# Kernel tuning notes

Measured on AMD Instinct MI355X. Metric: run time of the kernel, lower is better.

## Reference

```python
import jax, jax.numpy as jnp
import numpy as np

B, T, C, H, W = 2, 16, 128, 32, 32
D_STATE, D_CONV, EXPAND = 16, 4, 2
D_INNER = EXPAND * C           # 256
DT_RANK = (C + 15) // 16       # 8 (mamba default ceil(d_model/16))
HIDDEN = int(C * 4.0)          # mlp_ratio = 4
EPS = 1e-6


def setup_inputs() -> dict:
    key = jax.random.key(0)
    ks = jax.random.split(key, 10)
    f = lambda k, s, sc=0.02: jax.random.normal(k, s, jnp.float32) * sc
    return dict(
        x=jax.random.normal(ks[0], (B, T, C, H, W), jnp.float32),
        norm1_w=jnp.ones((C,), jnp.float32),
        in_proj_w=f(ks[1], (2 * D_INNER, C)),
        conv_w=f(ks[2], (D_INNER, D_CONV), 0.1),
        conv_b=jnp.zeros((D_INNER,), jnp.float32),
        x_proj_w=f(ks[3], (DT_RANK + 2 * D_STATE, D_INNER)),
        dt_proj_w=f(ks[4], (D_INNER, DT_RANK), 0.1),
        dt_proj_b=jnp.full((D_INNER,), -2.0, jnp.float32),
        A_log=jnp.log(jnp.tile(jnp.arange(1, D_STATE + 1, dtype=jnp.float32), (D_INNER, 1))),
        D_param=jnp.ones((D_INNER,), jnp.float32),
        out_proj_w=f(ks[5], (C, D_INNER)),
        norm2_w=jnp.ones((C,), jnp.float32),
        fc1_w=f(ks[6], (HIDDEN, C)),
        fc1_b=jnp.zeros((HIDDEN,), jnp.float32),
        fc2_w=f(ks[7], (C, HIDDEN)),
        fc2_b=jnp.zeros((C,), jnp.float32),
    )


def _rmsnorm(x, w):
    var = jnp.mean(x * x, axis=-1, keepdims=True)
    return w * (x * jax.lax.rsqrt(var + EPS))


def _mamba(x, in_proj_w, conv_w, conv_b, x_proj_w, dt_proj_w, dt_proj_b,
           A_log, D_param, out_proj_w):
    # x: [Bn, T, C]
    Bn, T_, _ = x.shape
    xz = jnp.einsum('btc,ec->bte', x, in_proj_w)        # [Bn,T,2*Di]
    xi, z = jnp.split(xz, 2, axis=-1)
    # causal depthwise conv1d over T (kernel size D_CONV)
    xp = jnp.pad(xi, ((0, 0), (D_CONV - 1, 0), (0, 0)))
    conv = conv_b + sum(xp[:, k:k + T_, :] * conv_w[:, k] for k in range(D_CONV))
    xc = jax.nn.silu(conv)                               # [Bn,T,Di]
    dbl = jnp.einsum('btd,ed->bte', xc, x_proj_w)
    dt, Bm, Cm = jnp.split(dbl, [DT_RANK, DT_RANK + D_STATE], axis=-1)
    dt = jax.nn.softplus(jnp.einsum('btr,dr->btd', dt, dt_proj_w) + dt_proj_b)
    A = -jnp.exp(A_log)                                  # [Di,S]

    def step(h, inp):
        dt_t, B_t, C_t, u_t = inp                        # [Bn,Di],[Bn,S],[Bn,S],[Bn,Di]
        dA = jnp.exp(dt_t[:, :, None] * A)               # [Bn,Di,S]
        h = h * dA + dt_t[:, :, None] * B_t[:, None, :] * u_t[:, :, None]
        y = jnp.einsum('bds,bs->bd', h, C_t) + D_param * u_t
        return h, y

    h0 = jnp.zeros((Bn, D_INNER, D_STATE), x.dtype)
    xs = (dt.transpose(1, 0, 2), Bm.transpose(1, 0, 2),
          Cm.transpose(1, 0, 2), xc.transpose(1, 0, 2))
    _, ys = jax.lax.scan(step, h0, xs)                   # [T,Bn,Di]
    y = ys.transpose(1, 0, 2) * jax.nn.silu(z)
    return jnp.einsum('btd,cd->btc', y, out_proj_w)


def reference(x, norm1_w, in_proj_w, conv_w, conv_b, x_proj_w, dt_proj_w,
              dt_proj_b, A_log, D_param, out_proj_w, norm2_w,
              fc1_w, fc1_b, fc2_w, fc2_b):
    Bb, Tt, Cc, Hh, Ww = x.shape
    x_t = x.transpose(0, 3, 4, 1, 2).reshape(Bb * Hh * Ww, Tt, Cc)
    x_norm = _rmsnorm(x_t, norm1_w)
    m_args = (in_proj_w, conv_w, conv_b, x_proj_w, dt_proj_w, dt_proj_b,
              A_log, D_param, out_proj_w)
    out_fwd = _mamba(x_norm, *m_args)
    out_bwd = jnp.flip(_mamba(jnp.flip(x_norm, 1), *m_args), 1)
    x_t = x_t + out_fwd + out_bwd
    h = jax.nn.gelu(jnp.einsum('btc,hc->bth', _rmsnorm(x_t, norm2_w), fc1_w) + fc1_b,
                    approximate=False)
    mlp_out = jnp.einsum('bth,ch->btc', h, fc2_w) + fc2_b
    x_t = x_t + mlp_out
    return x_t.reshape(Bb, Hh, Ww, Tt, Cc).transpose(0, 3, 4, 1, 2)
```

## Files before the change

kernel.cpp:

```cpp
#include <hip/hip_runtime.h>
#include <math.h>

#define TT   16
#define CC   128
#define DI   256
#define SS   16
#define RR   8
#define HID  512
#define HWW  1024
#define NB   2048
#define EPSF 1e-6f

#define OFF_INPROJ  0
#define OFF_XPROJ   65536
#define OFF_OUTPROJ 75776
#define OFF_FC1     108544
#define OFF_FC2     174080
#define W_TOTAL     239616

#define WSB_XCF  524288u
#define WSB_XCB  (524288u + 16777216u)
#define WSB_Z    (524288u + 33554432u)
#define WS_NEEDED (524288u + 50331648u)

using f32x4  = __attribute__((ext_vector_type(4))) float;
using short8 = __attribute__((ext_vector_type(8))) short;

#define MFMA(a, b, c) __builtin_amdgcn_mfma_f32_16x16x32_bf16((a), (b), (c), 0, 0, 0)

__device__ __forceinline__ float siluf(float x) {
    return x * __builtin_amdgcn_rcpf(1.0f + __expf(-x));
}
__device__ __forceinline__ float geluf(float x) {
    float y = 0.7978845608028654f * (x + 0.044715f * x * x * x);
    y = fminf(y, 15.f);
    float e = __expf(2.f * y);
    float t = (e - 1.f) * __builtin_amdgcn_rcpf(e + 1.f);
    return 0.5f * x * (1.f + t);
}
__device__ __forceinline__ short f2bf(float f) {
    unsigned u = __float_as_uint(f);
    u += 0x7fffu + ((u >> 16) & 1u);
    return (short)(u >> 16);
}
__device__ __forceinline__ float bf2f(short s) {
    return __uint_as_float(((unsigned)(unsigned short)s) << 16);
}
__device__ __forceinline__ void stbf(char* base, int row, int col, int rowbytes, float v) {
    int byte = (col * 2) ^ ((row & 7) << 4);
    *(short*)(base + row * rowbytes + byte) = f2bf(v);
}
__device__ __forceinline__ float ldbf(const char* base, int row, int col, int rowbytes) {
    int byte = (col * 2) ^ ((row & 7) << 4);
    return bf2f(*(const short*)(base + row * rowbytes + byte));
}
__device__ __forceinline__ short ldraw(const char* base, int row, int col, int rowbytes) {
    int byte = (col * 2) ^ ((row & 7) << 4);
    return *(const short*)(base + row * rowbytes + byte);
}
__device__ __forceinline__ short8 ldA(const char* base, int row, int kelem, int rowbytes) {
    int byte = (kelem * 2) ^ ((row & 7) << 4);
    return *(const short8*)(base + row * rowbytes + byte);
}
__device__ __forceinline__ short8 ldB(const short* base, int idx) {
    return *(const short8*)(base + idx);
}

__global__ __launch_bounds__(256)
void cvt_weights(const float* __restrict__ in_proj_w,
                 const float* __restrict__ x_proj_w,
                 const float* __restrict__ out_proj_w,
                 const float* __restrict__ fc1_w,
                 const float* __restrict__ fc2_w,
                 short* __restrict__ ws)
{
    int i4 = (blockIdx.x * 256 + threadIdx.x) * 4;
    if (i4 >= W_TOTAL) return;
    const float* src;
    int off;
    if      (i4 < OFF_XPROJ)   { src = in_proj_w;  off = OFF_INPROJ;  }
    else if (i4 < OFF_OUTPROJ) { src = x_proj_w;   off = OFF_XPROJ;   }
    else if (i4 < OFF_FC1)     { src = out_proj_w; off = OFF_OUTPROJ; }
    else if (i4 < OFF_FC2)     { src = fc1_w;      off = OFF_FC1;     }
    else                       { src = fc2_w;      off = OFF_FC2;     }
    float4 v = *(const float4*)(src + (i4 - off));
    short4 o;
    o.x = f2bf(v.x); o.y = f2bf(v.y); o.z = f2bf(v.z); o.w = f2bf(v.w);
    *(short4*)(ws + i4) = o;
}

__global__ __launch_bounds__(256, 6)
void ka_front(const float* __restrict__ x,
              const float* __restrict__ norm1_w,
              const float* __restrict__ conv_w,
              const float* __restrict__ conv_b,
              const short* __restrict__ bw_in,
              short* __restrict__ xcf_g,
              short* __restrict__ xcb_g,
              short* __restrict__ z_g)
{
    __shared__ __align__(16) char lds[20480];
    char* A0 = lds;
    char* A1 = lds + 8192;
    char* A2 = lds + 12288;

    const int tid  = threadIdx.x;
    const int lane = tid & 63, wave = tid >> 6;
    const int mrow = lane & 15, kgrp = lane >> 4;
    const int n  = ((blockIdx.x & 7) << 8) | (blockIdx.x >> 3);
    const int b  = n >> 10, hw = n & 1023;
    const float* xin = x + (size_t)b * TT * CC * HWW + hw;

    {
        float* sX = (float*)A0;
        #pragma unroll
        for (int i = 0; i < 8; ++i) { int idx = tid + i * 256; sX[idx] = xin[(size_t)idx * HWW]; }
    }
    __syncthreads();
    {
        const float* sX = (const float*)A0;
        const int row = tid >> 4, l16 = tid & 15;
        float v[8]; float ssum = 0.f;
        #pragma unroll
        for (int k = 0; k < 8; ++k) { v[k] = sX[row * CC + l16 + 16 * k]; ssum += v[k] * v[k]; }
        ssum += __shfl_xor(ssum, 1); ssum += __shfl_xor(ssum, 2);
        ssum += __shfl_xor(ssum, 4); ssum += __shfl_xor(ssum, 8);
        const float rstd = __builtin_amdgcn_rsqf(ssum * (1.0f / CC) + EPSF);
        #pragma unroll
        for (int k = 0; k < 8; ++k) {
            int c = l16 + 16 * k;
            stbf(A1, row, c, 256, v[k] * rstd * norm1_w[c]);
        }
    }
    __syncthreads();
    {
        short8 aF[4];
        #pragma unroll
        for (int k = 0; k < 4; ++k) aF[k] = ldA(A1, mrow, k * 32 + kgrp * 8, 256);
        char* dst = (wave < 2) ? A0 : A2;
        const int n_w = wave * 128;
        #pragma unroll
        for (int q = 0; q < 4; ++q) {
            const int c0 = n_w + q * 32 + mrow;
            short8 b0[4], b1[4];
            #pragma unroll
            for (int k = 0; k < 4; ++k) b0[k] = ldB(bw_in, c0 * CC + kgrp * 8 + k * 32);
            #pragma unroll
            for (int k = 0; k < 4; ++k) b1[k] = ldB(bw_in, (c0 + 16) * CC + kgrp * 8 + k * 32);
            f32x4 a0 = (f32x4){0.f, 0.f, 0.f, 0.f};
            f32x4 a1 = (f32x4){0.f, 0.f, 0.f, 0.f};
            #pragma unroll
            for (int k = 0; k < 4; ++k) { a0 = MFMA(aF[k], b0[k], a0); a1 = MFMA(aF[k], b1[k], a1); }
            const int cl0 = c0 & 255, cl1 = (c0 + 16) & 255;
            #pragma unroll
            for (int r = 0; r < 4; ++r) {
                stbf(dst, kgrp * 4 + r, cl0, 512, a0[r]);
                stbf(dst, kgrp * 4 + r, cl1, 512, a1[r]);
            }
        }
    }
    __syncthreads();
    {
        const int ch = tid;
        float xi_r[TT];
        #pragma unroll
        for (int t = 0; t < TT; ++t) xi_r[t] = ldbf(A0, t, ch, 512);
        const float4 cw = *(const float4*)(conv_w + ch * 4);
        const float  cb = conv_b[ch];
        short* xf = xcf_g + n * 4096 + ch;
        short* xb = xcb_g + n * 4096 + ch;
        short* zo = z_g   + n * 4096 + ch;
        #pragma unroll
        for (int t = 0; t < TT; ++t) {
            float vf = fmaf(cw.w, xi_r[t], cb);
            if (t >= 1) vf = fmaf(cw.z, xi_r[t - 1], vf);
            if (t >= 2) vf = fmaf(cw.y, xi_r[t - 2], vf);
            if (t >= 3) vf = fmaf(cw.x, xi_r[t - 3], vf);
            xf[t * 256] = f2bf(siluf(vf));
            float vb = fmaf(cw.w, xi_r[15 - t], cb);
            if (t >= 1) vb = fmaf(cw.z, xi_r[16 - t], vb);
            if (t >= 2) vb = fmaf(cw.y, xi_r[17 - t], vb);
            if (t >= 3) vb = fmaf(cw.x, xi_r[18 - t], vb);
            xb[t * 256] = f2bf(siluf(vb));
            zo[t * 256] = ldraw(A2, t, ch, 512);
        }
    }
}

__global__ __launch_bounds__(256, 5)
void kb_scan(const float* __restrict__ dt_proj_w,
             const float* __restrict__ dt_proj_b,
             const float* __restrict__ D_param,
             const short* __restrict__ bw_xp,
             short* __restrict__ xcf_g,
             short* __restrict__ xcb_g,
             const short* __restrict__ z_g)
{
    __shared__ __align__(16) char lds[19456];
    char*  L0 = lds;
    char*  L1 = lds + 8192;
    float* SD = (float*)(lds + 16384);

    const int tid  = threadIdx.x;
    const int lane = tid & 63, wave = tid >> 6;
    const int mrow = lane & 15, kgrp = lane >> 4;
    const int dir = blockIdx.x & 1;
    const int bsw = blockIdx.x >> 1;
    const int n = ((bsw & 7) << 8) | (bsw >> 3);
    short* xcn = (dir ? xcb_g : xcf_g) + n * 4096;
    const short* zn = z_g + n * 4096;

    {
        #pragma unroll
        for (int p = 0; p < 2; ++p) {
            int i8 = tid + p * 256;
            int e = i8 * 8, row = e >> 8, col = e & 255;
            short8 v = *(const short8*)(xcn + e);
            short8 w = *(const short8*)(zn + e);
            int byte = (col * 2) ^ ((row & 7) << 4);
            *(short8*)(L0 + row * 512 + byte) = v;
            *(short8*)(L1 + row * 512 + byte) = w;
        }
    }
    __syncthreads();
    {
        if (wave < 3) {
            const int col  = wave * 16 + mrow;
            const int colc = (col < 40) ? col : 39;
            short8 bF[8];
            #pragma unroll
            for (int k = 0; k < 8; ++k) bF[k] = ldB(bw_xp, colc * DI + k * 32 + kgrp * 8);
            f32x4 aE = (f32x4){0.f, 0.f, 0.f, 0.f};
            f32x4 aO = (f32x4){0.f, 0.f, 0.f, 0.f};
            #pragma unroll
            for (int k = 0; k < 4; ++k) {
                aE = MFMA(ldA(L0, mrow, (2 * k)     * 32 + kgrp * 8, 512), bF[2 * k],     aE);
                aO = MFMA(ldA(L0, mrow, (2 * k + 1) * 32 + kgrp * 8, 512), bF[2 * k + 1], aO);
            }
            if (col < 40) {
                #pragma unroll
                for (int r = 0; r < 4; ++r) SD[(kgrp * 4 + r) * 40 + col] = aE[r] + aO[r];
            }
        }
    }
    __syncthreads();
    {
        const int ch = tid;
        float dtw[RR];
        {
            float4 w0 = *(const float4*)(dt_proj_w + ch * RR);
            float4 w1 = *(const float4*)(dt_proj_w + ch * RR + 4);
            dtw[0] = w0.x; dtw[1] = w0.y; dtw[2] = w0.z; dtw[3] = w0.w;
            dtw[4] = w1.x; dtw[5] = w1.y; dtw[6] = w1.z; dtw[7] = w1.w;
        }
        const float db_ = dt_proj_b[ch];
        const float Dp  = D_param[ch];
        float u[TT];
        #pragma unroll
        for (int t = 0; t < TT; ++t) u[t] = ldbf(L0, t, ch, 512);
        float h[SS];
        #pragma unroll
        for (int s = 0; s < SS; ++s) h[s] = 0.f;
        #pragma unroll
        for (int t = 0; t < TT; ++t) {
            float xr = db_;
            #pragma unroll
            for (int r = 0; r < RR; ++r) xr = fmaf(dtw[r], SD[t * 40 + r], xr);
            const float e  = __expf(xr);
            const float dt = (xr > 15.f) ? xr : __logf(1.f + e);
            const int   to = dir ? (15 - t) : t;
            const float zv = ldbf(L1, to, ch, 512);
            float dA[SS];
            dA[0] = __builtin_amdgcn_rcpf(1.f + e);
            #pragma unroll
            for (int i = 1; i < SS; ++i) dA[i] = dA[(i - 1) >> 1] * dA[i >> 1];
            const float bu = dt * u[t];
            float y = 0.f;
            #pragma unroll
            for (int sg = 0; sg < 4; ++sg) {
                f32x4 B4 = *(const f32x4*)(SD + t * 40 + 8  + sg * 4);
                f32x4 C4 = *(const f32x4*)(SD + t * 40 + 24 + sg * 4);
                h[sg*4+0] = fmaf(h[sg*4+0], dA[sg*4+0], B4[0] * bu); y = fmaf(h[sg*4+0], C4[0], y);
                h[sg*4+1] = fmaf(h[sg*4+1], dA[sg*4+1], B4[1] * bu); y = fmaf(h[sg*4+1], C4[1], y);
                h[sg*4+2] = fmaf(h[sg*4+2], dA[sg*4+2], B4[2] * bu); y = fmaf(h[sg*4+2], C4[2], y);
                h[sg*4+3] = fmaf(h[sg*4+3], dA[sg*4+3], B4[3] * bu); y = fmaf(h[sg*4+3], C4[3], y);
            }
            y = fmaf(Dp, u[t], y) * siluf(zv);
            xcn[t * 256 + ch] = f2bf(y);
        }
    }
}

__global__ __launch_bounds__(256, 4)
void kc_back2(const float* __restrict__ x,
              const float* __restrict__ norm2_w,
              const float* __restrict__ fc1_b,
              const float* __restrict__ fc2_b,
              const short* __restrict__ bw,
              const short* __restrict__ yf_g,
              const short* __restrict__ yb_g,
              float* __restrict__ out)
{
    __shared__ __align__(16) char lds[40960];
    float* X2 = (float*)lds;
    char*  A1 = lds + 16384;
    char*  H  = lds + 24576;

    const short* bw_op = bw + OFF_OUTPROJ;
    const short* bw_f1 = bw + OFF_FC1;
    const short* bw_f2 = bw + OFF_FC2;

    const int tid  = threadIdx.x;
    const int lane = tid & 63, wave = tid >> 6;
    const int mrow = lane & 15, kgrp = lane >> 4;
    const int bsw = ((blockIdx.x & 7) << 7) | (blockIdx.x >> 3);
    const int n0 = bsw * 2, n1 = n0 + 1;
    const int b0 = n0 >> 10, hw0 = n0 & 1023;
    const int b1 = n1 >> 10, hw1 = n1 & 1023;
    const float* xin0 = x + (size_t)b0 * TT * CC * HWW + hw0;
    const float* xin1 = x + (size_t)b1 * TT * CC * HWW + hw1;
    float* oout0 = out + (size_t)b0 * TT * CC * HWW + hw0;
    float* oout1 = out + (size_t)b1 * TT * CC * HWW + hw1;

    float* X2A = X2;
    float* X2B = X2 + 2048;
    const int c0 = wave * 32 + mrow;
    const int c1 = c0 + 16;

    {
        float xrA[8], xrB[8];
        #pragma unroll
        for (int r = 0; r < 4; ++r) {
            const int row = kgrp * 4 + r;
            xrA[r]     = xin0[(size_t)(row * CC + c0) * HWW];
            xrA[4 + r] = xin0[(size_t)(row * CC + c1) * HWW];
            xrB[r]     = xin1[(size_t)(row * CC + c0) * HWW];
            xrB[4 + r] = xin1[(size_t)(row * CC + c1) * HWW];
        }
        const short* yfA = yf_g + n0 * 4096;
        const short* yfB = yf_g + n1 * 4096;
        const short* ybA = yb_g + n0 * 4096;
        const short* ybB = yb_g + n1 * 4096;
        f32x4 a0A = (f32x4){0.f,0.f,0.f,0.f}, a1A = a0A, a0B = a0A, a1B = a0A;
        #pragma unroll 2
        for (int kk = 0; kk < 8; ++kk) {
            const int ko = kk * 32 + kgrp * 8;
            short8 bF0 = ldB(bw_op, c0 * DI + ko);
            short8 bF1 = ldB(bw_op, c1 * DI + ko);
            short8 fA = *(const short8*)(yfA + mrow * 256 + ko);
            short8 fB = *(const short8*)(yfB + mrow * 256 + ko);
            short8 gA = *(const short8*)(ybA + (15 - mrow) * 256 + ko);
            short8 gB = *(const short8*)(ybB + (15 - mrow) * 256 + ko);
            a0A = MFMA(fA, bF0, a0A); a0A = MFMA(gA, bF0, a0A);
            a1A = MFMA(fA, bF1, a1A); a1A = MFMA(gA, bF1, a1A);
            a0B = MFMA(fB, bF0, a0B); a0B = MFMA(gB, bF0, a0B);
            a1B = MFMA(fB, bF1, a1B); a1B = MFMA(gB, bF1, a1B);
        }
        #pragma unroll
        for (int r = 0; r < 4; ++r) {
            const int row = kgrp * 4 + r;
            X2A[row * CC + c0] = a0A[r] + xrA[r];
            X2A[row * CC + c1] = a1A[r] + xrA[4 + r];
            X2B[row * CC + c0] = a0B[r] + xrB[r];
            X2B[row * CC + c1] = a1B[r] + xrB[4 + r];
        }
    }
    __syncthreads();

    {
        const int row = tid >> 3;
        const int s   = row >> 4;
        const int r16 = row & 15;
        const int l8  = tid & 7;
        const float* Xs = X2 + s * 2048;
        float v[16]; float ssum = 0.f;
        #pragma unroll
        for (int k = 0; k < 16; ++k) { v[k] = Xs[r16 * CC + l8 + 8 * k]; ssum += v[k] * v[k]; }
        ssum += __shfl_xor(ssum, 1); ssum += __shfl_xor(ssum, 2); ssum += __shfl_xor(ssum, 4);
        const float rstd = __builtin_amdgcn_rsqf(ssum * (1.0f / CC) + EPSF);
        char* A1s = A1 + s * 4096;
        #pragma unroll
        for (int k = 0; k < 16; ++k) {
            int c = l8 + 8 * k;
            stbf(A1s, r16, c, 256, v[k] * rstd * norm2_w[c]);
        }
    }
    __syncthreads();

    {
        short8 aFA[4], aFB[4];
        #pragma unroll
        for (int k = 0; k < 4; ++k) {
            aFA[k] = ldA(A1,        mrow, k * 32 + kgrp * 8, 256);
            aFB[k] = ldA(A1 + 4096, mrow, k * 32 + kgrp * 8, 256);
        }
        f32x4 o0A = (f32x4){0.f,0.f,0.f,0.f}, o1A = o0A, o0B = o0A, o1B = o0A;
        #pragma unroll
        for (int hh = 0; hh < 2; ++hh) {
            #pragma unroll
            for (int q = 0; q < 2; ++q) {
                const int cc0 = hh * 256 + wave * 64 + q * 32 + mrow;
                const int cc1 = cc0 + 16;
                f32x4 h0A = (f32x4){0.f,0.f,0.f,0.f}, h1A = h0A, h0B = h0A, h1B = h0A;
                #pragma unroll
                for (int k = 0; k < 4; ++k) {
                    short8 b0 = ldB(bw_f1, cc0 * CC + kgrp * 8 + k * 32);
                    short8 b1 = ldB(bw_f1, cc1 * CC + kgrp * 8 + k * 32);
                    h0A = MFMA(aFA[k], b0, h0A); h1A = MFMA(aFA[k], b1, h1A);
                    h0B = MFMA(aFB[k], b0, h0B); h1B = MFMA(aFB[k], b1, h1B);
                }
                const float bb0 = fc1_b[cc0], bb1 = fc1_b[cc1];
                const int cl0 = cc0 & 255, cl1 = cc1 & 255;
                #pragma unroll
                for (int r = 0; r < 4; ++r) {
                    stbf(H,        kgrp * 4 + r, cl0, 512, geluf(h0A[r] + bb0));
                    stbf(H,        kgrp * 4 + r, cl1, 512, geluf(h1A[r] + bb1));
                    stbf(H + 8192, kgrp * 4 + r, cl0, 512, geluf(h0B[r] + bb0));
                    stbf(H + 8192, kgrp * 4 + r, cl1, 512, geluf(h1B[r] + bb1));
                }
            }
            __syncthreads();
            #pragma unroll 2
            for (int k = 0; k < 8; ++k) {
                const int ko = k * 32 + kgrp * 8;
                short8 b0 = ldB(bw_f2, c0 * HID + hh * 256 + ko);
                short8 b1 = ldB(bw_f2, c1 * HID + hh * 256 + ko);
                short8 aA = ldA(H,        mrow, ko, 512);
                short8 aB = ldA(H + 8192, mrow, ko, 512);
                o0A = MFMA(aA, b0, o0A); o1A = MFMA(aA, b1, o1A);
                o0B = MFMA(aB, b0, o0B); o1B = MFMA(aB, b1, o1B);
            }
            __syncthreads();
        }
        const float bb0 = fc2_b[c0], bb1 = fc2_b[c1];
        #pragma unroll
        for (int r = 0; r < 4; ++r) {
            const int row = kgrp * 4 + r;
            oout0[(size_t)(row * CC + c0) * HWW] = X2A[row * CC + c0] + o0A[r] + bb0;
            oout0[(size_t)(row * CC + c1) * HWW] = X2A[row * CC + c1] + o1A[r] + bb1;
            oout1[(size_t)(row * CC + c0) * HWW] = X2B[row * CC + c0] + o0B[r] + bb0;
            oout1[(size_t)(row * CC + c1) * HWW] = X2B[row * CC + c1] + o1B[r] + bb1;
        }
    }
}

template<int DIR>
__device__ __forceinline__ void scan_mono(const float* __restrict__ dbl,
                                          char* __restrict__ xcb,
                                          const char* __restrict__ zb,
                                          char* __restrict__ yb,
                                          const float* __restrict__ dtw,
                                          float db_, float Dp, int ch)
{
    float u[TT];
    #pragma unroll
    for (int t = 0; t < TT; ++t) u[t] = ldbf(xcb, t, ch, 512);
    float h[SS];
    #pragma unroll
    for (int s = 0; s < SS; ++s) h[s] = 0.f;
    #pragma unroll
    for (int t = 0; t < TT; ++t) {
        float xr = db_;
        #pragma unroll
        for (int r = 0; r < RR; ++r) xr = fmaf(dtw[r], dbl[t * 40 + r], xr);
        const float e  = __expf(xr);
        const float dt = (xr > 15.f) ? xr : __logf(1.f + e);
        const int   to = DIR ? (15 - t) : t;
        const float zv = ldbf(zb, to, ch, 512);
        float dA[SS];
        dA[0] = __builtin_amdgcn_rcpf(1.f + e);
        #pragma unroll
        for (int i = 1; i < SS; ++i) dA[i] = dA[(i - 1) >> 1] * dA[i >> 1];
        const float bu = dt * u[t];
        float y = 0.f;
        #pragma unroll
        for (int sg = 0; sg < 4; ++sg) {
            float4 B4 = *(const float4*)(dbl + t * 40 + 8  + sg * 4);
            float4 C4 = *(const float4*)(dbl + t * 40 + 24 + sg * 4);
            h[sg*4+0] = fmaf(h[sg*4+0], dA[sg*4+0], B4.x * bu); y = fmaf(h[sg*4+0], C4.x, y);
            h[sg*4+1] = fmaf(h[sg*4+1], dA[sg*4+1], B4.y * bu); y = fmaf(h[sg*4+1], C4.y, y);
            h[sg*4+2] = fmaf(h[sg*4+2], dA[sg*4+2], B4.z * bu); y = fmaf(h[sg*4+2], C4.z, y);
            h[sg*4+3] = fmaf(h[sg*4+3], dA[sg*4+3], B4.w * bu); y = fmaf(h[sg*4+3], C4.w, y);
        }
        y = fmaf(Dp, u[t], y) * siluf(zv);
        if (DIR == 0) stbf(xcb, t,  ch, 512, y);
        else          stbf(yb,  to, ch, 512, y);
    }
}

__global__ __launch_bounds__(512, 4)
void tmb_mono(const float* __restrict__ x,
              const float* __restrict__ norm1_w,
              const float* __restrict__ conv_w,
              const float* __restrict__ conv_b,
              const float* __restrict__ dt_proj_w,
              const float* __restrict__ dt_proj_b,
              const float* __restrict__ D_param,
              const float* __restrict__ norm2_w,
              const float* __restrict__ fc1_b,
              const float* __restrict__ fc2_b,
              const short* __restrict__ bw,
              float* __restrict__ out)
{
    __shared__ __align__(16) char lds[40960];
    char* A0  = lds;
    char* A2  = lds + 8192;
    char* A3  = lds + 16384;
    char* A4f = lds + 24576;
    char* A4b = lds + 32768;

    const short* bw_in = bw + OFF_INPROJ;
    const short* bw_xp = bw + OFF_XPROJ;
    const short* bw_op = bw + OFF_OUTPROJ;
    const short* bw_f1 = bw + OFF_FC1;
    const short* bw_f2 = bw + OFF_FC2;

    const int tid  = threadIdx.x;
    const int team = tid >> 8;
    const int ch   = tid & 255;
    const int lane = tid & 63;
    const int wave = tid >> 6;
    const int mrow = lane & 15;
    const int kgrp = lane >> 4;

    const int n  = ((blockIdx.x & 7) << 8) | (blockIdx.x >> 3);
    const int b  = n >> 10;
    const int hw = n & 1023;
    const float* xin  = x   + (size_t)b * TT * CC * HWW + hw;
    float*       oout = out + (size_t)b * TT * CC * HWW + hw;

    {
        float* sX = (float*)A0;
        #pragma unroll
        for (int i = 0; i < 4; ++i) { int idx = tid + i * 512; sX[idx] = xin[(size_t)idx * HWW]; }
    }
    __syncthreads();
    float res[4];
    {
        const float* sX = (const float*)A0;
        #pragma unroll
        for (int i = 0; i < 4; ++i) res[i] = sX[tid + i * 512];
    }
    {
        const float* sX = (const float*)A0;
        const int row = tid >> 5, l32 = tid & 31;
        float v[4]; float ssum = 0.f;
        #pragma unroll
        for (int k = 0; k < 4; ++k) { v[k] = sX[row * CC + l32 + 32 * k]; ssum += v[k] * v[k]; }
        ssum += __shfl_xor(ssum, 1); ssum += __shfl_xor(ssum, 2);
        ssum += __shfl_xor(ssum, 4); ssum += __shfl_xor(ssum, 8); ssum += __shfl_xor(ssum, 16);
        const float rstd = __builtin_amdgcn_rsqf(ssum * (1.0f / CC) + EPSF);
        #pragma unroll
        for (int k = 0; k < 4; ++k) { int c = l32 + 32 * k; stbf(A4f, row, c, 256, v[k] * rstd * norm1_w[c]); }
    }
    __syncthreads();
    {
        short8 aF[4];
        #pragma unroll
        for (int k = 0; k < 4; ++k) aF[k] = ldA(A4f, mrow, k * 32 + kgrp * 8, 256);
        const int n_w = wave * 64;
        short8 bX[8], bY[8];
        #pragma unroll
        for (int i = 0; i < 8; ++i) { const int tile = i >> 2, k = i & 3; bX[i] = ldB(bw_in, (n_w + tile * 16 + mrow) * CC + kgrp * 8 + k * 32); }
        #pragma unroll
        for (int i = 0; i < 8; ++i) { const int tile = 2 + (i >> 2), k = i & 3; bY[i] = ldB(bw_in, (n_w + tile * 16 + mrow) * CC + kgrp * 8 + k * 32); }
        f32x4 acc[4];
        #pragma unroll
        for (int i = 0; i < 4; ++i) acc[i] = (f32x4){0.f, 0.f, 0.f, 0.f};
        #pragma unroll
        for (int i = 0; i < 8; ++i) acc[i >> 2]       = MFMA(aF[i & 3], bX[i], acc[i >> 2]);
        #pragma unroll
        for (int i = 0; i < 8; ++i) acc[2 + (i >> 2)] = MFMA(aF[i & 3], bY[i], acc[2 + (i >> 2)]);
        char* dst = (wave < 4) ? A2 : A3;
        #pragma unroll
        for (int tile = 0; tile < 4; ++tile) {
            const int cl = (n_w + tile * 16 + mrow) & 255;
            #pragma unroll
            for (int r = 0; r < 4; ++r) stbf(dst, kgrp * 4 + r, cl, 512, acc[tile][r]);
        }
    }
    __syncthreads();
    {
        float xi_r[TT];
        #pragma unroll
        for (int t = 0; t < TT; ++t) xi_r[t] = ldbf(A2, t, ch, 512);
        const float4 cw = *(const float4*)(conv_w + ch * 4);
        const float  cb = conv_b[ch];
        char* dst = team ? A4b : A4f;
        if (team == 0) {
            #pragma unroll
            for (int t = 0; t < TT; ++t) {
                float vf = fmaf(cw.w, xi_r[t], cb);
                if (t >= 1) vf = fmaf(cw.z, xi_r[t - 1], vf);
                if (t >= 2) vf = fmaf(cw.y, xi_r[t - 2], vf);
                if (t >= 3) vf = fmaf(cw.x, xi_r[t - 3], vf);
                stbf(dst, t, ch, 512, siluf(vf));
            }
        } else {
            #pragma unroll
            for (int t = 0; t < TT; ++t) {
                float vb = fmaf(cw.w, xi_r[15 - t], cb);
                if (t >= 1) vb = fmaf(cw.z, xi_r[16 - t], vb);
                if (t >= 2) vb = fmaf(cw.y, xi_r[17 - t], vb);
                if (t >= 3) vb = fmaf(cw.x, xi_r[18 - t], vb);
                stbf(dst, t, ch, 512, siluf(vb));
            }
        }
    }
    __syncthreads();
    float* SDBL = (float*)A0;
    {
        const int wv = wave & 3;
        if (wv < 3) {
            const char* src = team ? A4b : A4f;
            float* db = SDBL + team * 640;
            const int col  = wv * 16 + mrow;
            const int colc = (col < 40) ? col : 39;
            const int wp = colc * DI + kgrp * 8;
            short8 bF[8];
            #pragma unroll
            for (int k = 0; k < 8; ++k) bF[k] = ldB(bw_xp, wp + k * 32);
            f32x4 accE = (f32x4){0.f, 0.f, 0.f, 0.f};
            f32x4 accO = (f32x4){0.f, 0.f, 0.f, 0.f};
            #pragma unroll
            for (int k = 0; k < 4; ++k) {
                accE = MFMA(ldA(src, mrow, (2*k)   * 32 + kgrp * 8, 512), bF[2*k],   accE);
                accO = MFMA(ldA(src, mrow, (2*k+1) * 32 + kgrp * 8, 512), bF[2*k+1], accO);
            }
            if (col < 40) {
                #pragma unroll
                for (int r = 0; r < 4; ++r) db[(kgrp * 4 + r) * 40 + col] = accE[r] + accO[r];
            }
        }
    }
    __syncthreads();
    {
        float dtw[RR];
        float4 w0 = *(const float4*)(dt_proj_w + ch * RR);
        float4 w1 = *(const float4*)(dt_proj_w + ch * RR + 4);
        dtw[0] = w0.x; dtw[1] = w0.y; dtw[2] = w0.z; dtw[3] = w0.w;
        dtw[4] = w1.x; dtw[5] = w1.y; dtw[6] = w1.z; dtw[7] = w1.w;
        const float db_ = dt_proj_b[ch];
        const float Dp  = D_param[ch];
        if (team == 0) scan_mono<0>(SDBL,       A4f, A3, A4f, dtw, db_, Dp, ch);
        else           scan_mono<1>(SDBL + 640, A4b, A3, A2,  dtw, db_, Dp, ch);
    }
    __syncthreads();
    {
        const int col = wave * 16 + mrow;
        short8 bF[8];
        #pragma unroll
        for (int k = 0; k < 8; ++k) bF[k] = ldB(bw_op, col * DI + k * 32 + kgrp * 8);
        f32x4 accE = (f32x4){0.f, 0.f, 0.f, 0.f};
        f32x4 accO = (f32x4){0.f, 0.f, 0.f, 0.f};
        #pragma unroll
        for (int k = 0; k < 4; ++k) {
            accE = MFMA(ldA(A4f, mrow, (2*k)   * 32 + kgrp * 8, 512), bF[2*k],   accE);
            accO = MFMA(ldA(A4f, mrow, (2*k+1) * 32 + kgrp * 8, 512), bF[2*k+1], accO);
        }
        #pragma unroll
        for (int k = 0; k < 4; ++k) {
            accE = MFMA(ldA(A2, mrow, (2*k)   * 32 + kgrp * 8, 512), bF[2*k],   accE);
            accO = MFMA(ldA(A2, mrow, (2*k+1) * 32 + kgrp * 8, 512), bF[2*k+1], accO);
        }
        float* O = (float*)A3;
        #pragma unroll
        for (int r = 0; r < 4; ++r) O[(kgrp * 4 + r) * CC + col] = accE[r] + accO[r];
    }
    __syncthreads();
    {
        const float* O  = (const float*)A3;
        float*       X2 = (float*)A0;
        #pragma unroll
        for (int i = 0; i < 4; ++i) { int idx = tid + i * 512; X2[idx] = res[i] + O[idx]; }
    }
    __syncthreads();
    {
        const float* sX = (const float*)A0;
        const int row = tid >> 5, l32 = tid & 31;
        float v[4]; float ssum = 0.f;
        #pragma unroll
        for (int k = 0; k < 4; ++k) { v[k] = sX[row * CC + l32 + 32 * k]; ssum += v[k] * v[k]; }
        ssum += __shfl_xor(ssum, 1); ssum += __shfl_xor(ssum, 2);
        ssum += __shfl_xor(ssum, 4); ssum += __shfl_xor(ssum, 8); ssum += __shfl_xor(ssum, 16);
        const float rstd = __builtin_amdgcn_rsqf(ssum * (1.0f / CC) + EPSF);
        #pragma unroll
        for (int k = 0; k < 4; ++k) { int c = l32 + 32 * k; stbf(A4f, row, c, 256, v[k] * rstd * norm2_w[c]); }
    }
    __syncthreads();
    {
        short8 aF[4];
        #pragma unroll
        for (int k = 0; k < 4; ++k) aF[k] = ldA(A4f, mrow, k * 32 + kgrp * 8, 256);
        const int n_w = wave * 64;
        short8 bX[8], bY[8];
        #pragma unroll
        for (int i = 0; i < 8; ++i) { const int tile = i >> 2, k = i & 3; bX[i] = ldB(bw_f1, (n_w + tile * 16 + mrow) * CC + kgrp * 8 + k * 32); }
        #pragma unroll
        for (int i = 0; i < 8; ++i) { const int tile = 2 + (i >> 2), k = i & 3; bY[i] = ldB(bw_f1, (n_w + tile * 16 + mrow) * CC + kgrp * 8 + k * 32); }
        f32x4 acc[4];
        #pragma unroll
        for (int i = 0; i < 4; ++i) acc[i] = (f32x4){0.f, 0.f, 0.f, 0.f};
        #pragma unroll
        for (int i = 0; i < 8; ++i) acc[i >> 2]       = MFMA(aF[i & 3], bX[i], acc[i >> 2]);
        #pragma unroll
        for (int i = 0; i < 8; ++i) acc[2 + (i >> 2)] = MFMA(aF[i & 3], bY[i], acc[2 + (i >> 2)]);
        char* dst = (wave < 4) ? A2 : A3;
        #pragma unroll
        for (int tile = 0; tile < 4; ++tile) {
            const int col = n_w + tile * 16 + mrow;
            const float b1 = fc1_b[col];
            const int cl = col & 255;
            #pragma unroll
            for (int r = 0; r < 4; ++r) stbf(dst, kgrp * 4 + r, cl, 512, geluf(acc[tile][r] + b1));
        }
    }
    __syncthreads();
    {
        const int col = wave * 16 + mrow;
        short8 bX[8], bY[8];
        #pragma unroll
        for (int k = 0; k < 8; ++k) bX[k] = ldB(bw_f2, col * HID + k * 32 + kgrp * 8);
        #pragma unroll
        for (int k = 0; k < 8; ++k) bY[k] = ldB(bw_f2, col * HID + (8 + k) * 32 + kgrp * 8);
        f32x4 accE = (f32x4){0.f, 0.f, 0.f, 0.f};
        f32x4 accO = (f32x4){0.f, 0.f, 0.f, 0.f};
        #pragma unroll
        for (int k = 0; k < 8; ++k) {
            accE = MFMA(ldA(A2, mrow, k * 32 + kgrp * 8, 512), bX[k], accE);
            accO = MFMA(ldA(A3, mrow, k * 32 + kgrp * 8, 512), bY[k], accO);
        }
        const float* X2 = (const float*)A0;
        const float bb = fc2_b[col];
        #pragma unroll
        for (int r = 0; r < 4; ++r) {
            const int t = kgrp * 4 + r;
            oout[(size_t)(t * CC + col) * HWW] = X2[t * CC + col] + accE[r] + accO[r] + bb;
        }
    }
}

extern "C" void kernel_launch(void* const* d_in, const int* in_sizes, int n_in,
                              void* d_out, int out_size, void* d_ws, size_t ws_size,
                              hipStream_t stream) {
    (void)in_sizes; (void)n_in; (void)out_size;
    short* bw = (short*)d_ws;
    cvt_weights<<<dim3((W_TOTAL / 4 + 255) / 256), dim3(256), 0, stream>>>(
        (const float*)d_in[2],  (const float*)d_in[5],  (const float*)d_in[10],
        (const float*)d_in[12], (const float*)d_in[14], bw);

    if (ws_size >= (size_t)WS_NEEDED) {
        short* xcf = (short*)((char*)d_ws + WSB_XCF);
        short* xcb = (short*)((char*)d_ws + WSB_XCB);
        short* zg  = (short*)((char*)d_ws + WSB_Z);
        ka_front<<<dim3(NB), dim3(256), 0, stream>>>(
            (const float*)d_in[0], (const float*)d_in[1], (const float*)d_in[3],
            (const float*)d_in[4], bw + OFF_INPROJ, xcf, xcb, zg);
        kb_scan<<<dim3(NB * 2), dim3(256), 0, stream>>>(
            (const float*)d_in[6], (const float*)d_in[7], (const float*)d_in[9],
            bw + OFF_XPROJ, xcf, xcb, zg);
        kc_back2<<<dim3(NB / 2), dim3(256), 0, stream>>>(
            (const float*)d_in[0], (const float*)d_in[11], (const float*)d_in[13],
            (const float*)d_in[15], bw, xcf, xcb, (float*)d_out);
    } else {
        tmb_mono<<<dim3(NB), dim3(512), 0, stream>>>(
            (const float*)d_in[0],  (const float*)d_in[1],  (const float*)d_in[3],
            (const float*)d_in[4],  (const float*)d_in[6],  (const float*)d_in[7],
            (const float*)d_in[9],  (const float*)d_in[11], (const float*)d_in[13],
            (const float*)d_in[15], bw, (float*)d_out);
    }
}
```

Measured before the change: 181.6 us.

## Stage residual and output in contiguous workspace, add tiled transpose kernel for output

The front kernel now also writes the raw input per sequence into a contiguous fp32 workspace buffer. The back kernel reads the residual from that buffer instead of doing strided gathers, and writes its result contiguously into a buffer that reuses the z region. A new LDS-tiled transpose kernel then scatters that buffer into the final strided output layout with coalesced float4 accesses. The goal is to replace strided global reads and writes with coalesced ones, at the cost of extra workspace traffic and one more kernel launch; the scan kernel's block-to-direction mapping is also reordered.

```diff
diff --git a/kernel.cpp b/kernel.cpp
--- a/kernel.cpp
+++ b/kernel.cpp
@@ -18,10 +18,12 @@
 #define OFF_FC2     174080
 #define W_TOTAL     239616
 
-#define WSB_XCF  524288u
-#define WSB_XCB  (524288u + 16777216u)
-#define WSB_Z    (524288u + 33554432u)
-#define WS_NEEDED (524288u + 50331648u)
+#define WSB_XCF   524288u
+#define WSB_XCB   (524288u + 16777216u)
+#define WSB_ZXO   (524288u + 33554432u)
+#define WSB_XRES  (524288u + 50331648u)
+#define WS_T1     (524288u + 50331648u)
+#define WS_T2     (524288u + 67108864u)
 
 using f32x4  = __attribute__((ext_vector_type(4))) float;
 using short8 = __attribute__((ext_vector_type(8))) short;
@@ -89,6 +91,7 @@
     *(short4*)(ws + i4) = o;
 }
 
+template<int XRES>
 __global__ __launch_bounds__(256, 6)
 void ka_front(const float* __restrict__ x,
               const float* __restrict__ norm1_w,
@@ -97,7 +100,8 @@
               const short* __restrict__ bw_in,
               short* __restrict__ xcf_g,
               short* __restrict__ xcb_g,
-              short* __restrict__ z_g)
+              short* __restrict__ z_g,
+              float* __restrict__ xres_g)
 {
     __shared__ __align__(16) char lds[20480];
     char* A0 = lds;
@@ -114,7 +118,12 @@
     {
         float* sX = (float*)A0;
         #pragma unroll
-        for (int i = 0; i < 8; ++i) { int idx = tid + i * 256; sX[idx] = xin[(size_t)idx * HWW]; }
+        for (int i = 0; i < 8; ++i) {
+            int idx = tid + i * 256;
+            float v = xin[(size_t)idx * HWW];
+            sX[idx] = v;
+            if (XRES) xres_g[(size_t)n * 2048 + idx] = v;
+        }
     }
     __syncthreads();
     {
@@ -204,8 +213,8 @@
     const int tid  = threadIdx.x;
     const int lane = tid & 63, wave = tid >> 6;
     const int mrow = lane & 15, kgrp = lane >> 4;
-    const int dir = blockIdx.x & 1;
-    const int bsw = blockIdx.x >> 1;
+    const int dir = blockIdx.x >> 11;
+    const int bsw = blockIdx.x & 2047;
     const int n = ((bsw & 7) << 8) | (bsw >> 3);
     short* xcn = (dir ? xcb_g : xcf_g) + n * 4096;
     const short* zn = z_g + n * 4096;
@@ -291,15 +300,17 @@
     }
 }
 
+template<int XRES>
 __global__ __launch_bounds__(256, 4)
 void kc_back2(const float* __restrict__ x,
+              const float* __restrict__ xres,
               const float* __restrict__ norm2_w,
               const float* __restrict__ fc1_b,
               const float* __restrict__ fc2_b,
               const short* __restrict__ bw,
               const short* __restrict__ yf_g,
               const short* __restrict__ yb_g,
-              float* __restrict__ out)
+              float* __restrict__ xout)
 {
     __shared__ __align__(16) char lds[40960];
     float* X2 = (float*)lds;
@@ -319,8 +330,8 @@
     const int b1 = n1 >> 10, hw1 = n1 & 1023;
     const float* xin0 = x + (size_t)b0 * TT * CC * HWW + hw0;
     const float* xin1 = x + (size_t)b1 * TT * CC * HWW + hw1;
-    float* oout0 = out + (size_t)b0 * TT * CC * HWW + hw0;
-    float* oout1 = out + (size_t)b1 * TT * CC * HWW + hw1;
+    float* xoA = xout + (size_t)n0 * 2048;
+    float* xoB = xout + (size_t)n1 * 2048;
 
     float* X2A = X2;
     float* X2B = X2 + 2048;
@@ -329,13 +340,26 @@
 
     {
         float xrA[8], xrB[8];
-        #pragma unroll
-        for (int r = 0; r < 4; ++r) {
-            const int row = kgrp * 4 + r;
-            xrA[r]     = xin0[(size_t)(row * CC + c0) * HWW];
-            xrA[4 + r] = xin0[(size_t)(row * CC + c1) * HWW];
-            xrB[r]     = xin1[(size_t)(row * CC + c0) * HWW];
-            xrB[4 + r] = xin1[(size_t)(row * CC + c1) * HWW];
+        if (XRES) {
+            const float* rA = xres + (size_t)n0 * 2048;
+            const float* rB = xres + (size_t)n1 * 2048;
+            #pragma unroll
+            for (int r = 0; r < 4; ++r) {
+                const int row = kgrp * 4 + r;
+                xrA[r]     = rA[row * CC + c0];
+                xrA[4 + r] = rA[row * CC + c1];
+                xrB[r]     = rB[row * CC + c0];
+                xrB[4 + r] = rB[row * CC + c1];
+            }
+        } else {
+            #pragma unroll
+            for (int r = 0; r < 4; ++r) {
+                const int row = kgrp * 4 + r;
+                xrA[r]     = xin0[(size_t)(row * CC + c0) * HWW];
+                xrA[4 + r] = xin0[(size_t)(row * CC + c1) * HWW];
+                xrB[r]     = xin1[(size_t)(row * CC + c0) * HWW];
+                xrB[4 + r] = xin1[(size_t)(row * CC + c1) * HWW];
+            }
         }
         const short* yfA = yf_g + n0 * 4096;
         const short* yfB = yf_g + n1 * 4096;
@@ -436,11 +460,50 @@
         #pragma unroll
         for (int r = 0; r < 4; ++r) {
             const int row = kgrp * 4 + r;
-            oout0[(size_t)(row * CC + c0) * HWW] = X2A[row * CC + c0] + o0A[r] + bb0;
-            oout0[(size_t)(row * CC + c1) * HWW] = X2A[row * CC + c1] + o1A[r] + bb1;
-            oout1[(size_t)(row * CC + c0) * HWW] = X2B[row * CC + c0] + o0B[r] + bb0;
-            oout1[(size_t)(row * CC + c1) * HWW] = X2B[row * CC + c1] + o1B[r] + bb1;
-        }
+            xoA[row * CC + c0] = X2A[row * CC + c0] + o0A[r] + bb0;
+            xoA[row * CC + c1] = X2A[row * CC + c1] + o1A[r] + bb1;
+            xoB[row * CC + c0] = X2B[row * CC + c0] + o0B[r] + bb0;
+            xoB[row * CC + c1] = X2B[row * CC + c1] + o1B[r] + bb1;
+        }
+    }
+}
+
+__global__ __launch_bounds__(256, 2)
+void kt_out(const float* __restrict__ xout, float* __restrict__ out)
+{
+    __shared__ float T[32 * 260];
+    const int id  = blockIdx.x;
+    const int b   = id >> 8;
+    const int rem = id & 255;
+    const int tcT = rem >> 2;
+    const int hwT = rem & 3;
+    const int tc0 = tcT * 32;
+    const int hw0 = hwT * 256;
+    const int tid = threadIdx.x;
+    const int hwl = tid >> 3;
+    const int tc4 = (tid & 7) * 4;
+    #pragma unroll
+    for (int p = 0; p < 8; ++p) {
+        const int hwp = p * 32 + hwl;
+        float4 v = *(const float4*)(xout + (size_t)(b * 1024 + hw0 + hwp) * 2048 + tc0 + tc4);
+        T[(tc4 + 0) * 260 + hwp] = v.x;
+        T[(tc4 + 1) * 260 + hwp] = v.y;
+        T[(tc4 + 2) * 260 + hwp] = v.z;
+        T[(tc4 + 3) * 260 + hwp] = v.w;
+    }
+    __syncthreads();
+    const int tcl = tid >> 3;
+    const int o   = (tid & 7) * 4;
+    float* orow = out + (size_t)(b * 2048 + tc0 + tcl) * 1024 + hw0;
+    #pragma unroll
+    for (int i = 0; i < 8; ++i) {
+        const int hwp = i * 32 + o;
+        float4 v;
+        v.x = T[tcl * 260 + hwp + 0];
+        v.y = T[tcl * 260 + hwp + 1];
+        v.z = T[tcl * 260 + hwp + 2];
+        v.w = T[tcl * 260 + hwp + 3];
+        *(float4*)(orow + hwp) = v;
     }
 }
 
@@ -749,19 +812,35 @@
         (const float*)d_in[2],  (const float*)d_in[5],  (const float*)d_in[10],
         (const float*)d_in[12], (const float*)d_in[14], bw);
 
-    if (ws_size >= (size_t)WS_NEEDED) {
-        short* xcf = (short*)((char*)d_ws + WSB_XCF);
-        short* xcb = (short*)((char*)d_ws + WSB_XCB);
-        short* zg  = (short*)((char*)d_ws + WSB_Z);
-        ka_front<<<dim3(NB), dim3(256), 0, stream>>>(
-            (const float*)d_in[0], (const float*)d_in[1], (const float*)d_in[3],
-            (const float*)d_in[4], bw + OFF_INPROJ, xcf, xcb, zg);
+    if (ws_size >= (size_t)WS_T1) {
+        short* xcf  = (short*)((char*)d_ws + WSB_XCF);
+        short* xcb  = (short*)((char*)d_ws + WSB_XCB);
+        short* zg   = (short*)((char*)d_ws + WSB_ZXO);
+        float* xout = (float*)((char*)d_ws + WSB_ZXO);
+        float* xres = (float*)((char*)d_ws + WSB_XRES);
+        const int tier2 = (ws_size >= (size_t)WS_T2);
+        if (tier2) {
+            ka_front<1><<<dim3(NB), dim3(256), 0, stream>>>(
+                (const float*)d_in[0], (const float*)d_in[1], (const float*)d_in[3],
+                (const float*)d_in[4], bw + OFF_INPROJ, xcf, xcb, zg, xres);
+        } else {
+            ka_front<0><<<dim3(NB), dim3(256), 0, stream>>>(
+                (const float*)d_in[0], (const float*)d_in[1], (const float*)d_in[3],
+                (const float*)d_in[4], bw + OFF_INPROJ, xcf, xcb, zg, xres);
+        }
         kb_scan<<<dim3(NB * 2), dim3(256), 0, stream>>>(
             (const float*)d_in[6], (const float*)d_in[7], (const float*)d_in[9],
             bw + OFF_XPROJ, xcf, xcb, zg);
-        kc_back2<<<dim3(NB / 2), dim3(256), 0, stream>>>(
-            (const float*)d_in[0], (const float*)d_in[11], (const float*)d_in[13],
-            (const float*)d_in[15], bw, xcf, xcb, (float*)d_out);
+        if (tier2) {
+            kc_back2<1><<<dim3(NB / 2), dim3(256), 0, stream>>>(
+                (const float*)d_in[0], xres, (const float*)d_in[11], (const float*)d_in[13],
+                (const float*)d_in[15], bw, xcf, xcb, xout);
+        } else {
+            kc_back2<0><<<dim3(NB / 2), dim3(256), 0, stream>>>(
+                (const float*)d_in[0], xres, (const float*)d_in[11], (const float*)d_in[13],
+                (const float*)d_in[15], bw, xcf, xcb, xout);
+        }
+        kt_out<<<dim3(512), dim3(256), 0, stream>>>(xout, (float*)d_out);
     } else {
         tmb_mono<<<dim3(NB), dim3(512), 0, stream>>>(
             (const float*)d_in[0],  (const float*)d_in[1],  (const float*)d_in[3],
```

After: 173.3 us. -4.6%, faster.
